# Kernel tuning notes

Measured on AMD Instinct MI355X. Metric: run time of the kernel, lower is better.

Reference implementation:

```python
import jax, jax.numpy as jnp
import numpy as np

N_NODES = 100000
K_HOPS = 2


def _gcn_norm(edge_index, edge_weight, num_nodes, fill_value=1.0):
    # renorm trick: add self-loops with weight fill_value, then D^-1/2 A D^-1/2
    row, col = edge_index[0], edge_index[1]
    sl = jnp.arange(num_nodes, dtype=edge_index.dtype)
    row = jnp.concatenate([row, sl])
    col = jnp.concatenate([col, sl])
    w = jnp.concatenate([edge_weight, jnp.full((num_nodes,), fill_value, edge_weight.dtype)])
    deg = jax.ops.segment_sum(w, row, num_segments=num_nodes)
    dinv = jnp.where(deg > 0, jax.lax.rsqrt(deg), 0.0)
    normed_w = dinv[row] * w * dinv[col]
    return row, col, normed_w


def setup_inputs() -> dict:
    key = jax.random.key(0)
    k1, k2, k3 = jax.random.split(key, 3)
    n_edges, d, units = 1000000, 64, 64
    x = jax.random.normal(k1, (N_NODES, d), dtype=jnp.float32)
    edge_index = jax.random.randint(k2, (2, n_edges), 0, N_NODES, dtype=jnp.int32)
    edge_weight = jnp.ones((n_edges,), dtype=jnp.float32)
    kernel = jax.random.normal(k3, (d, units), dtype=jnp.float32) * (1.0 / np.sqrt(d))
    bias = jnp.zeros((units,), dtype=jnp.float32)
    return {"x": x, "edge_index": edge_index, "edge_weight": edge_weight,
            "kernel": kernel, "bias": bias}


def reference(x, edge_index, edge_weight, kernel, bias):
    # SGC: K-hop normalized sparse propagation, then single dense linear
    row, col, w = _gcn_norm(edge_index, edge_weight, N_NODES, fill_value=1.0)
    h = x
    for _ in range(K_HOPS):
        h = jax.ops.segment_sum(w[:, None] * h[col], row, num_segments=N_NODES)
    out = h @ kernel + bias  # activation=None
    return out
```

## Files before the change

kernel.cpp:

```cpp
#include <hip/hip_runtime.h>


constexpr int kN = 100000;
constexpr int kD = 64;
constexpr int BSHIFT = 9;
constexpr int NBUCK = (kN + 511) >> BSHIFT;
constexpr int CHUNK = 4096;
constexpr int XW_ROWS = 128;

__device__ __forceinline__ float bf2f(unsigned short u) {
    return __uint_as_float(((unsigned)u) << 16);
}
__device__ __forceinline__ unsigned short f2bf(float f) {
    unsigned b = __float_as_uint(f);
    b += 0x7FFF + ((b >> 16) & 1);
    return (unsigned short)(b >> 16);
}

__global__ __launch_bounds__(256) void kA_count(const int* __restrict__ row,
                                                int* __restrict__ bc, int nblk, int E) {
    __shared__ int hist[256];
    int t = threadIdx.x;
    hist[t] = 0;
    __syncthreads();
    int g0 = blockIdx.x * CHUNK;
    int n = min(CHUNK, E - g0);
    for (int i = t; i < n; i += 256) {
        atomicAdd(&hist[row[g0 + i] >> BSHIFT], 1);
    }
    __syncthreads();
    if (t < NBUCK) bc[t * nblk + blockIdx.x] = hist[t];
}

__global__ __launch_bounds__(256) void kA_scanB(int* __restrict__ bc,
                                                int* __restrict__ tot, int nblk) {
    __shared__ int sh[256];
    int b = blockIdx.x;
    int t = threadIdx.x;
    int* p = bc + (size_t)b * nblk;
    int ipt = (nblk + 255) >> 8;
    int s0 = t * ipt;
    int s1 = min(s0 + ipt, nblk);
    int lsum = 0;
    for (int k = s0; k < s1; ++k) lsum += p[k];
    sh[t] = lsum;
    __syncthreads();
    for (int off = 1; off < 256; off <<= 1) {
        int add = (t >= off) ? sh[t - off] : 0;
        __syncthreads();
        sh[t] += add;
        __syncthreads();
    }
    int run = sh[t] - lsum;
    for (int k = s0; k < s1; ++k) {
        int v = p[k];
        p[k] = run;
        run += v;
    }
    if (t == 255) tot[b] = sh[255];
}

__global__ __launch_bounds__(256) void kA_scanT(const int* __restrict__ tot,
                                                int* __restrict__ base) {
    __shared__ int sh[256];
    int t = threadIdx.x;
    int v = (t < NBUCK) ? tot[t] : 0;
    sh[t] = v;
    __syncthreads();
    for (int off = 1; off < 256; off <<= 1) {
        int add = (t >= off) ? sh[t - off] : 0;
        __syncthreads();
        sh[t] += add;
        __syncthreads();
    }
    if (t < NBUCK) base[t] = sh[t] - v;
}

__global__ __launch_bounds__(256) void kA_place(const int* __restrict__ row,
                                                const int* __restrict__ col,
                                                const float* __restrict__ w,
                                                const int* __restrict__ bc,
                                                const int* __restrict__ base, int nblk,
                                                int2* __restrict__ tmp, int E) {
    __shared__ int hist[256];
    __shared__ int lbase[256];
    __shared__ int gb[256];
    __shared__ int cur[256];
    __shared__ int2 stage[CHUNK];
    __shared__ unsigned char bkt[CHUNK];
    int t = threadIdx.x;
    hist[t] = 0;
    __syncthreads();
    int g0 = blockIdx.x * CHUNK;
    int n = min(CHUNK, E - g0);
    for (int i = t; i < n; i += 256) {
        atomicAdd(&hist[row[g0 + i] >> BSHIFT], 1);
    }
    __syncthreads();
    int v = hist[t];
    lbase[t] = v;
    __syncthreads();
    for (int off = 1; off < 256; off <<= 1) {
        int add = (t >= off) ? lbase[t - off] : 0;
        __syncthreads();
        lbase[t] += add;
        __syncthreads();
    }
    int excl = lbase[t] - v;
    __syncthreads();
    lbase[t] = excl;
    cur[t] = excl;
    if (t < NBUCK) gb[t] = base[t] + bc[t * nblk + blockIdx.x];
    __syncthreads();
    for (int i = t; i < n; i += 256) {
        int r = row[g0 + i];
        int c = col[g0 + i];
        float wv = w[g0 + i];
        int b = r >> BSHIFT;
        int lp = atomicAdd(&cur[b], 1);
        stage[lp] = make_int2(c | ((r & 511) << 17), __float_as_int(wv));
        bkt[lp] = (unsigned char)b;
    }
    __syncthreads();
    for (int i = t; i < n; i += 256) {
        int b = bkt[i];
        tmp[gb[b] + (i - lbase[b])] = stage[i];
    }
}

__global__ __launch_bounds__(512) void kD_deg(const int2* __restrict__ tmp,
                                              const int* __restrict__ base,
                                              float* __restrict__ dinv, int E) {
    __shared__ float degs[512];
    int b = blockIdx.x;
    int t = threadIdx.x;
    degs[t] = 0.0f;
    __syncthreads();
    int gbase = base[b];
    int gend = (b == NBUCK - 1) ? E : base[b + 1];
    int node0 = b << BSHIFT;
    int nloc = min(512, kN - node0);
    for (int i = gbase + t; i < gend; i += 512) {
        int2 e = tmp[i];
        atomicAdd(&degs[(e.x >> 17) & 511], __int_as_float(e.y));
    }
    __syncthreads();
    if (t < nloc) {
        float d = 1.0f + degs[t];
        dinv[node0 + t] = (d > 0.0f) ? rsqrtf(d) : 0.0f;
    }
}

__global__ __launch_bounds__(512) void kB_sort(const int2* __restrict__ tmp,
                                               const int* __restrict__ base,
                                               const float* __restrict__ dinv,
                                               int2* __restrict__ ecw,
                                               int* __restrict__ start, int E) {
    __shared__ int hist[512];
    __shared__ int cur[512];
    int b = blockIdx.x;
    int t = threadIdx.x;
    int gbase = base[b];
    int gend = (b == NBUCK - 1) ? E : base[b + 1];
    int size = gend - gbase;
    int node0 = b << BSHIFT;
    int nloc = min(512, kN - node0);
    hist[t] = 0;
    __syncthreads();
    for (int i = t; i < size; i += 512) {
        atomicAdd(&hist[(tmp[gbase + i].x >> 17) & 511], 1);
    }
    __syncthreads();
    int v = hist[t];
    hist[t] = v;
    __syncthreads();
    for (int off = 1; off < 512; off <<= 1) {
        int add = (t >= off) ? hist[t - off] : 0;
        __syncthreads();
        hist[t] += add;
        __syncthreads();
    }
    int excl = hist[t] - v;
    __syncthreads();
    cur[t] = excl;
    __syncthreads();
    if (t < nloc) start[node0 + t] = gbase + excl;
    if (b == 0 && t == 0) start[kN] = E;
    for (int i = t; i < size; i += 512) {
        int2 e = tmp[gbase + i];
        int c = e.x & 0x1FFFF;
        int rl = (e.x >> 17) & 511;
        float wn = dinv[node0 + rl] * __int_as_float(e.y) * dinv[c];
        int lp = atomicAdd(&cur[rl], 1);
        ecw[gbase + lp] = make_int2(c << 7, __float_as_int(wn));
    }
}

__global__ __launch_bounds__(256) void k_xw(const float* __restrict__ x,
                                            const float* __restrict__ W,
                                            unsigned short* __restrict__ y, int n) {
    __shared__ float Xs[XW_ROWS][kD];
    int t = threadIdx.x;
    int lane = t & 63;
    int wv = t >> 6;
    int row0 = blockIdx.x * XW_ROWS;
    float Wc[kD];
#pragma unroll
    for (int k = 0; k < kD; ++k) Wc[k] = W[k * kD + lane];
    for (int i = t; i < XW_ROWS * (kD / 4); i += 256) {
        int r = i >> 4;
        int q = i & 15;
        float4 v = make_float4(0.0f, 0.0f, 0.0f, 0.0f);
        if (row0 + r < n)
            v = *reinterpret_cast<const float4*>(x + (size_t)(row0 + r) * kD + q * 4);
        *reinterpret_cast<float4*>(&Xs[r][q * 4]) = v;
    }
    __syncthreads();
    int rbase = wv * 32;
#pragma unroll
    for (int rr = 0; rr < 32; rr += 2) {
        int r0 = rbase + rr;
        float acc0 = 0.0f, acc1 = 0.0f;
#pragma unroll
        for (int q = 0; q < 16; ++q) {
            float4 a = *reinterpret_cast<const float4*>(&Xs[r0][q * 4]);
            float4 b = *reinterpret_cast<const float4*>(&Xs[r0 + 1][q * 4]);
            acc0 = fmaf(a.x, Wc[q * 4 + 0], acc0);
            acc1 = fmaf(b.x, Wc[q * 4 + 0], acc1);
            acc0 = fmaf(a.y, Wc[q * 4 + 1], acc0);
            acc1 = fmaf(b.y, Wc[q * 4 + 1], acc1);
            acc0 = fmaf(a.z, Wc[q * 4 + 2], acc0);
            acc1 = fmaf(b.z, Wc[q * 4 + 2], acc1);
            acc0 = fmaf(a.w, Wc[q * 4 + 3], acc0);
            acc1 = fmaf(b.w, Wc[q * 4 + 3], acc1);
        }
        int gr = row0 + r0;
        if (gr < n) y[(size_t)gr * kD + lane] = f2bf(acc0);
        if (gr + 1 < n) y[(size_t)(gr + 1) * kD + lane] = f2bf(acc1);
    }
}

template <typename OutWriter>
__device__ __forceinline__ void hop_body(const int* __restrict__ start,
                                         const int2* __restrict__ ecw,
                                         const float* __restrict__ dinv,
                                         const unsigned short* __restrict__ h_in,
                                         int n, OutWriter writeout) {
    int node = blockIdx.x * 4 + __builtin_amdgcn_readfirstlane(threadIdx.x >> 6);
    int lane = threadIdx.x & 63;
    if (node >= n) return;
    const char* hb = (const char*)h_in;
    int lo = lane << 1;
    float di = dinv[node];
    float self = bf2f(h_in[(size_t)node * kD + lane]);
    float acc = di * di * self;
    int s = start[node], e = start[node + 1];
    int em1 = e - 1;
    for (int j = s; j < e; j += 8) {
        int2 v0 = ecw[j];
        int2 v1 = ecw[min(j + 1, em1)];
        int2 v2 = ecw[min(j + 2, em1)];
        int2 v3 = ecw[min(j + 3, em1)];
        int2 v4 = ecw[min(j + 4, em1)];
        int2 v5 = ecw[min(j + 5, em1)];
        int2 v6 = ecw[min(j + 6, em1)];
        int2 v7 = ecw[min(j + 7, em1)];
        float g0 = bf2f(*(const unsigned short*)(hb + (unsigned)(v0.x + lo)));
        float g1 = bf2f(*(const unsigned short*)(hb + (unsigned)(v1.x + lo)));
        float g2 = bf2f(*(const unsigned short*)(hb + (unsigned)(v2.x + lo)));
        float g3 = bf2f(*(const unsigned short*)(hb + (unsigned)(v3.x + lo)));
        float g4 = bf2f(*(const unsigned short*)(hb + (unsigned)(v4.x + lo)));
        float g5 = bf2f(*(const unsigned short*)(hb + (unsigned)(v5.x + lo)));
        float g6 = bf2f(*(const unsigned short*)(hb + (unsigned)(v6.x + lo)));
        float g7 = bf2f(*(const unsigned short*)(hb + (unsigned)(v7.x + lo)));
        float w0 = __int_as_float(v0.y);
        float w1 = (j + 1 < e) ? __int_as_float(v1.y) : 0.0f;
        float w2 = (j + 2 < e) ? __int_as_float(v2.y) : 0.0f;
        float w3 = (j + 3 < e) ? __int_as_float(v3.y) : 0.0f;
        float w4 = (j + 4 < e) ? __int_as_float(v4.y) : 0.0f;
        float w5 = (j + 5 < e) ? __int_as_float(v5.y) : 0.0f;
        float w6 = (j + 6 < e) ? __int_as_float(v6.y) : 0.0f;
        float w7 = (j + 7 < e) ? __int_as_float(v7.y) : 0.0f;
        acc = fmaf(w0, g0, acc);
        acc = fmaf(w1, g1, acc);
        acc = fmaf(w2, g2, acc);
        acc = fmaf(w3, g3, acc);
        acc = fmaf(w4, g4, acc);
        acc = fmaf(w5, g5, acc);
        acc = fmaf(w6, g6, acc);
        acc = fmaf(w7, g7, acc);
    }
    writeout(node, lane, di, acc);
}

__global__ __launch_bounds__(256) void k_hop1(const int* __restrict__ start,
                                              const int2* __restrict__ ecw,
                                              const float* __restrict__ dinv,
                                              const unsigned short* __restrict__ h_in,
                                              unsigned short* __restrict__ h_out, int n) {
    hop_body(start, ecw, dinv, h_in, n,
             [=](int node, int lane, float di, float acc) {
                 h_out[(size_t)node * kD + lane] = f2bf(acc);
             });
}

__global__ __launch_bounds__(256) void k_hop2(const int* __restrict__ start,
                                              const int2* __restrict__ ecw,
                                              const float* __restrict__ dinv,
                                              const unsigned short* __restrict__ h_in,
                                              const float* __restrict__ bias,
                                              float* __restrict__ out, int n) {
    hop_body(start, ecw, dinv, h_in, n,
             [=](int node, int lane, float di, float acc) {
                 __builtin_nontemporal_store(acc + bias[lane],
                                             &out[(size_t)node * kD + lane]);
             });
}

extern "C" void kernel_launch(void* const* d_in, const int* in_sizes, int n_in,
                              void* d_out, int out_size, void* d_ws, size_t ws_size,
                              hipStream_t stream) {
    const float* x    = (const float*)d_in[0];
    const int*   ei   = (const int*)d_in[1];
    const float* ew   = (const float*)d_in[2];
    const float* W    = (const float*)d_in[3];
    const float* bias = (const float*)d_in[4];
    const int E = in_sizes[1] / 2;
    const int* row = ei;
    const int* col = ei + E;

    const int nblk = (E + CHUNK - 1) / CHUNK;

    char* ws = (char*)d_ws;
    auto alloc = [&](size_t bytes) {
        char* p = ws;
        ws += ((bytes + 1023) & ~(size_t)1023);
        return p;
    };
    int*            base  = (int*)alloc(sizeof(int) * 256);
    int*            tot   = (int*)alloc(sizeof(int) * 256);
    int*            bc    = (int*)alloc(sizeof(int) * (size_t)NBUCK * nblk);
    int*            start = (int*)alloc(sizeof(int) * (kN + 1));
    float*          dinv  = (float*)alloc(sizeof(float) * kN);
    int2*           ecw   = (int2*)alloc(sizeof(int2) * (size_t)E);
    unsigned short* y     = (unsigned short*)alloc(sizeof(short) * (size_t)kN * kD);
    unsigned short* h1    = (unsigned short*)alloc(sizeof(short) * (size_t)kN * kD);
    int2*           tmp   = (int2*)h1;

    k_xw<<<(kN + XW_ROWS - 1) / XW_ROWS, 256, 0, stream>>>(x, W, y, kN);

    kA_count<<<nblk, 256, 0, stream>>>(row, bc, nblk, E);
    kA_scanB<<<NBUCK, 256, 0, stream>>>(bc, tot, nblk);
    kA_scanT<<<1, 256, 0, stream>>>(tot, base);
    kA_place<<<nblk, 256, 0, stream>>>(row, col, ew, bc, base, nblk, tmp, E);
    kD_deg<<<NBUCK, 512, 0, stream>>>(tmp, base, dinv, E);
    kB_sort<<<NBUCK, 512, 0, stream>>>(tmp, base, dinv, ecw, start, E);

    k_hop1<<<(kN + 3) / 4, 256, 0, stream>>>(start, ecw, dinv, y, h1, kN);
    k_hop2<<<(kN + 3) / 4, 256, 0, stream>>>(start, ecw, dinv, h1, bias,
                                             (float*)d_out, kN);
}
```

Before: 149.3 us.

## Process two nodes per wavefront with 32-bit paired bf16 gathers in hop kernels

Measured after the change: 141.7 us. 5.1% less time.

```diff
diff --git a/kernel.cpp b/kernel.cpp
--- a/kernel.cpp
+++ b/kernel.cpp
@@ -246,61 +246,59 @@
                                          const float* __restrict__ dinv,
                                          const unsigned short* __restrict__ h_in,
                                          int n, OutWriter writeout) {
-    int node = blockIdx.x * 4 + __builtin_amdgcn_readfirstlane(threadIdx.x >> 6);
+    int wv = threadIdx.x >> 6;
     int lane = threadIdx.x & 63;
-    if (node >= n) return;
+    int half = lane >> 5;
+    int sub = lane & 31;
+    int node = blockIdx.x * 8 + wv * 2 + half;
+    bool valid = node < n;
+    int nd = valid ? node : (n - 1);
     const char* hb = (const char*)h_in;
-    int lo = lane << 1;
-    float di = dinv[node];
-    float self = bf2f(h_in[(size_t)node * kD + lane]);
-    float acc = di * di * self;
-    int s = start[node], e = start[node + 1];
-    int em1 = e - 1;
-    for (int j = s; j < e; j += 8) {
-        int2 v0 = ecw[j];
+    int lo = sub << 2;
+    float di = dinv[nd];
+    unsigned su = *(const unsigned*)(hb + ((size_t)nd << 7) + lo);
+    float d2 = di * di;
+    float acc0 = d2 * __uint_as_float(su << 16);
+    float acc1 = d2 * __uint_as_float(su & 0xffff0000u);
+    int s = start[nd], e = start[nd + 1];
+    int d = e - s;
+    int dmax = max(d, __shfl_xor(d, 32));
+    int em1 = max(e - 1, 0);
+    for (int it = 0; it < dmax; it += 4) {
+        int j = s + it;
+        int2 v0 = ecw[min(j + 0, em1)];
         int2 v1 = ecw[min(j + 1, em1)];
         int2 v2 = ecw[min(j + 2, em1)];
         int2 v3 = ecw[min(j + 3, em1)];
-        int2 v4 = ecw[min(j + 4, em1)];
-        int2 v5 = ecw[min(j + 5, em1)];
-        int2 v6 = ecw[min(j + 6, em1)];
-        int2 v7 = ecw[min(j + 7, em1)];
-        float g0 = bf2f(*(const unsigned short*)(hb + (unsigned)(v0.x + lo)));
-        float g1 = bf2f(*(const unsigned short*)(hb + (unsigned)(v1.x + lo)));
-        float g2 = bf2f(*(const unsigned short*)(hb + (unsigned)(v2.x + lo)));
-        float g3 = bf2f(*(const unsigned short*)(hb + (unsigned)(v3.x + lo)));
-        float g4 = bf2f(*(const unsigned short*)(hb + (unsigned)(v4.x + lo)));
-        float g5 = bf2f(*(const unsigned short*)(hb + (unsigned)(v5.x + lo)));
-        float g6 = bf2f(*(const unsigned short*)(hb + (unsigned)(v6.x + lo)));
-        float g7 = bf2f(*(const unsigned short*)(hb + (unsigned)(v7.x + lo)));
-        float w0 = __int_as_float(v0.y);
-        float w1 = (j + 1 < e) ? __int_as_float(v1.y) : 0.0f;
-        float w2 = (j + 2 < e) ? __int_as_float(v2.y) : 0.0f;
-        float w3 = (j + 3 < e) ? __int_as_float(v3.y) : 0.0f;
-        float w4 = (j + 4 < e) ? __int_as_float(v4.y) : 0.0f;
-        float w5 = (j + 5 < e) ? __int_as_float(v5.y) : 0.0f;
-        float w6 = (j + 6 < e) ? __int_as_float(v6.y) : 0.0f;
-        float w7 = (j + 7 < e) ? __int_as_float(v7.y) : 0.0f;
-        acc = fmaf(w0, g0, acc);
-        acc = fmaf(w1, g1, acc);
-        acc = fmaf(w2, g2, acc);
-        acc = fmaf(w3, g3, acc);
-        acc = fmaf(w4, g4, acc);
-        acc = fmaf(w5, g5, acc);
-        acc = fmaf(w6, g6, acc);
-        acc = fmaf(w7, g7, acc);
-    }
-    writeout(node, lane, di, acc);
+        unsigned g0 = *(const unsigned*)(hb + (unsigned)(v0.x + lo));
+        unsigned g1 = *(const unsigned*)(hb + (unsigned)(v1.x + lo));
+        unsigned g2 = *(const unsigned*)(hb + (unsigned)(v2.x + lo));
+        unsigned g3 = *(const unsigned*)(hb + (unsigned)(v3.x + lo));
+        float w0 = (it + 0 < d) ? __int_as_float(v0.y) : 0.0f;
+        float w1 = (it + 1 < d) ? __int_as_float(v1.y) : 0.0f;
+        float w2 = (it + 2 < d) ? __int_as_float(v2.y) : 0.0f;
+        float w3 = (it + 3 < d) ? __int_as_float(v3.y) : 0.0f;
+        acc0 = fmaf(w0, __uint_as_float(g0 << 16), acc0);
+        acc1 = fmaf(w0, __uint_as_float(g0 & 0xffff0000u), acc1);
+        acc0 = fmaf(w1, __uint_as_float(g1 << 16), acc0);
+        acc1 = fmaf(w1, __uint_as_float(g1 & 0xffff0000u), acc1);
+        acc0 = fmaf(w2, __uint_as_float(g2 << 16), acc0);
+        acc1 = fmaf(w2, __uint_as_float(g2 & 0xffff0000u), acc1);
+        acc0 = fmaf(w3, __uint_as_float(g3 << 16), acc0);
+        acc1 = fmaf(w3, __uint_as_float(g3 & 0xffff0000u), acc1);
+    }
+    if (valid) writeout(node, sub, acc0, acc1);
 }
 
 __global__ __launch_bounds__(256) void k_hop1(const int* __restrict__ start,
                                               const int2* __restrict__ ecw,
                                               const float* __restrict__ dinv,
                                               const unsigned short* __restrict__ h_in,
-                                              unsigned short* __restrict__ h_out, int n) {
+                                              unsigned* __restrict__ h_out32, int n) {
     hop_body(start, ecw, dinv, h_in, n,
-             [=](int node, int lane, float di, float acc) {
-                 h_out[(size_t)node * kD + lane] = f2bf(acc);
+             [=](int node, int sub, float a0, float a1) {
+                 unsigned p = (unsigned)f2bf(a0) | ((unsigned)f2bf(a1) << 16);
+                 h_out32[((size_t)node << 5) + sub] = p;
              });
 }
 
@@ -311,9 +309,10 @@
                                               const float* __restrict__ bias,
                                               float* __restrict__ out, int n) {
     hop_body(start, ecw, dinv, h_in, n,
-             [=](int node, int lane, float di, float acc) {
-                 __builtin_nontemporal_store(acc + bias[lane],
-                                             &out[(size_t)node * kD + lane]);
+             [=](int node, int sub, float a0, float a1) {
+                 float2 b = *reinterpret_cast<const float2*>(bias + 2 * sub);
+                 float2 o = make_float2(a0 + b.x, a1 + b.y);
+                 *reinterpret_cast<float2*>(out + ((size_t)node << 6) + 2 * sub) = o;
              });
 }
 
@@ -356,7 +355,8 @@
     kD_deg<<<NBUCK, 512, 0, stream>>>(tmp, base, dinv, E);
     kB_sort<<<NBUCK, 512, 0, stream>>>(tmp, base, dinv, ecw, start, E);
 
-    k_hop1<<<(kN + 3) / 4, 256, 0, stream>>>(start, ecw, dinv, y, h1, kN);
-    k_hop2<<<(kN + 3) / 4, 256, 0, stream>>>(start, ecw, dinv, h1, bias,
+    k_hop1<<<(kN + 7) / 8, 256, 0, stream>>>(start, ecw, dinv, y,
+                                             (unsigned*)h1, kN);
+    k_hop2<<<(kN + 7) / 8, 256, 0, stream>>>(start, ecw, dinv, h1, bias,
                                              (float*)d_out, kN);
 }
```
